# Kernel tuning notes

Measured on AMD Instinct MI355X. Metric: run time of the kernel, lower is better.

The kernel has to match this reference:

```python
import jax, jax.numpy as jnp
import numpy as np

B, S, C, D, K = 8, 1024, 8192, 256, 512
FREEDOM = 0.1

def setup_inputs() -> dict:
    key = jax.random.key(0)
    k1, k2, k3 = jax.random.split(key, 3)
    concept_seq = jax.random.uniform(k1, (B, S, C), dtype=jnp.float32)
    concept_emb = jax.random.uniform(k2, (C, D), dtype=jnp.float32)  # nn.Parameter(torch.rand(max_c+1, d_model))
    centroid_emb = jax.random.uniform(k3, (K, D), dtype=jnp.float32)
    return {"concept_seq": concept_seq, "concept_emb": concept_emb,
            "centroid_emb": centroid_emb, "domain": 0}

def reference(concept_seq, concept_emb, centroid_emb, domain):
    # normalize multi-hot rows by their count (rows summing to 0 use count=1)
    cnt = jnp.sum(concept_seq, axis=-1, keepdims=True)
    cnt = jnp.where(cnt == 0, jnp.ones_like(cnt), cnt)
    cs = concept_seq / cnt
    # weighted embedding sum: [B,S,C] @ [C,D] -> [B,S,D]
    e_free = jnp.einsum('bsc,cd->bsd', cs, concept_emb)
    # nearest centroid (argmin of cdist == argmin of squared distance)
    flat = e_free.reshape(-1, D)                               # [B*S, D]
    d2 = (jnp.sum(flat * flat, axis=1, keepdims=True)
          - 2.0 * flat @ centroid_emb.T
          + jnp.sum(centroid_emb * centroid_emb, axis=1))      # [B*S, K]
    idx = jnp.argmin(d2, axis=1)                               # [B*S]
    e_cent = centroid_emb[idx].reshape(e_free.shape)           # [B,S,D]
    return e_free * FREEDOM + e_cent * (1.0 - FREEDOM)
```

## Files before the change

kernel.cpp:

```cpp
#include <hip/hip_runtime.h>


typedef unsigned short u16;
typedef unsigned int   u32;
using bf16x8 = __attribute__((ext_vector_type(8))) short;
using f32x4  = __attribute__((ext_vector_type(4))) float;

#define MFMA_B16(A,B,C) __builtin_amdgcn_mfma_f32_16x16x32_bf16((A),(B),(C),0,0,0)

static __device__ __forceinline__ u16 f2bf(float f){
  u32 u = __builtin_bit_cast(u32, f);
  u += 0x7FFFu + ((u >> 16) & 1u);
  return (u16)(u >> 16);
}
static __device__ __forceinline__ float bf2f(u16 h){
  u32 u = ((u32)h) << 16;
  return __builtin_bit_cast(float, u);
}
static __device__ __forceinline__ void split2(float va, float vb, u32& hw, u32& lw){
  u16 ha = f2bf(va), hb = f2bf(vb);
  hw = (u32)ha | ((u32)hb << 16);
  lw = (u32)f2bf(va - bf2f(ha)) | ((u32)f2bf(vb - bf2f(hb)) << 16);
}

#define SZ_PART    (4UL*8192UL*256UL*4UL)
#define OFF_CNT    (SZ_PART)
#define SZ_CNT     (4UL*8192UL*4UL)
#define OFF_BHI    (OFF_CNT + SZ_CNT)
#define SZ_BHI     (8192UL*256UL*2UL)
#define OFF_BLO    (OFF_BHI + SZ_BHI)
#define OFF_CTHI   (OFF_BLO + SZ_BHI)
#define SZ_CT      (512UL*256UL*2UL)
#define OFF_CTLO   (OFF_CTHI + SZ_CT)
#define OFF_CNORM  (OFF_CTLO + SZ_CT)

__global__ __launch_bounds__(256) void ce_prep(
    const float* __restrict__ emb, const float* __restrict__ cent,
    u16* __restrict__ Bhi, u16* __restrict__ Blo,
    u16* __restrict__ CThi, u16* __restrict__ CTlo,
    double* __restrict__ cnormd)
{
  const int b = blockIdx.x, t = threadIdx.x;
  const int l = t & 63;
  const int lr = l & 15, lk = l >> 4;
  if (b < 1024) {
    const int g  = b * 4 + (t >> 6);
    const int nt = g >> 8, ksg = g & 255;
    u32 hw[4], lw[4];
    #pragma unroll
    for (int p = 0; p < 4; ++p) {
      float va = emb[(size_t)(ksg*32 + lk*8 + 2*p    )*256 + nt*16 + lr];
      float vb = emb[(size_t)(ksg*32 + lk*8 + 2*p + 1)*256 + nt*16 + lr];
      split2(va, vb, hw[p], lw[p]);
    }
    const size_t fi = ((size_t)nt*256 + ksg)*64 + l;
    *(uint4*)(Bhi + fi*8) = make_uint4(hw[0],hw[1],hw[2],hw[3]);
    *(uint4*)(Blo + fi*8) = make_uint4(lw[0],lw[1],lw[2],lw[3]);
  } else if (b < 1088) {
    const int g  = (b - 1024) * 4 + (t >> 6);
    const int nt = g >> 3, ksg = g & 7;
    u32 hw[4], lw[4];
    #pragma unroll
    for (int p = 0; p < 4; ++p) {
      float va = cent[(size_t)(nt*16 + lr)*256 + ksg*32 + lk*8 + 2*p    ] - 0.5f;
      float vb = cent[(size_t)(nt*16 + lr)*256 + ksg*32 + lk*8 + 2*p + 1] - 0.5f;
      split2(va, vb, hw[p], lw[p]);
    }
    const size_t fi = ((size_t)nt*8 + ksg)*64 + l;
    *(uint4*)(CThi + fi*8) = make_uint4(hw[0],hw[1],hw[2],hw[3]);
    *(uint4*)(CTlo + fi*8) = make_uint4(lw[0],lw[1],lw[2],lw[3]);
  } else {
    const int row = (b - 1088)*8 + (t >> 5);
    const int h = t & 31;
    double s = 0.0;
    #pragma unroll
    for (int j = 0; j < 8; ++j) {
      float x = cent[(size_t)row*256 + h*8 + j] - 0.5f;
      s += (double)x * (double)x;
    }
    #pragma unroll
    for (int off = 16; off > 0; off >>= 1) s += __shfl_xor(s, off);
    if (h == 0) cnormd[row] = s;
  }
}

__global__ __launch_bounds__(512) void ce_gemm(
    const float* __restrict__ seq,
    const u16* __restrict__ Bhi, const u16* __restrict__ Blo,
    float* __restrict__ part, float* __restrict__ cntpart)
{
  __shared__ char Ah[128*128];
  __shared__ char Al[128*128];
  __shared__ float cred[128][4];

  const int t   = threadIdx.x;
  const int blk = blockIdx.x;
  const int mt  = blk >> 2;
  const int ks  = blk & 3;
  const size_t rowBase = (size_t)mt * 128;
  const int ar  = t >> 2;
  const int ac4 = t & 3;
  const float* aptr = seq + (rowBase + ar) * 8192 + (size_t)ks * 2048 + ac4 * 16;

  const int w = t >> 6, l = t & 63;
  const int wm = w >> 2, wn = w & 3;
  const int lr = l & 15, lk = l >> 4;

  f32x4 acc[4][4];
  #pragma unroll
  for (int i = 0; i < 4; ++i)
    #pragma unroll
    for (int j = 0; j < 4; ++j) acc[i][j] = (f32x4){0.f,0.f,0.f,0.f};

  float csum = 0.f;
  float4 areg[4];
  #pragma unroll
  for (int i = 0; i < 4; ++i) areg[i] = *(const float4*)(aptr + i*4);

  for (int step = 0; step < 32; ++step) {
    __syncthreads();
    const int ksg0 = ks*64 + step*2;
    bf16x8 bh[2][4], bl[2][4];
    #pragma unroll
    for (int ksub = 0; ksub < 2; ++ksub)
      #pragma unroll
      for (int ni = 0; ni < 4; ++ni) {
        const size_t fi = (((size_t)(wn*4 + ni))*256 + (ksg0 + ksub))*64 + l;
        bh[ksub][ni] = *(const bf16x8*)(Bhi + fi*8);
        bl[ksub][ni] = *(const bf16x8*)(Blo + fi*8);
      }
    float v[16];
    #pragma unroll
    for (int i = 0; i < 4; ++i) {
      v[4*i] = areg[i].x; v[4*i+1] = areg[i].y; v[4*i+2] = areg[i].z; v[4*i+3] = areg[i].w;
    }
    #pragma unroll
    for (int i = 0; i < 16; ++i) csum += v[i];
    #pragma unroll
    for (int chunk = 0; chunk < 2; ++chunk) {
      u32 hw[4], lw[4];
      #pragma unroll
      for (int p = 0; p < 4; ++p) split2(v[chunk*8 + 2*p], v[chunk*8 + 2*p + 1], hw[p], lw[p]);
      const int slot = ac4*2 + chunk;
      const int off  = ar*128 + ((slot ^ (ar & 7)) << 4);
      *(uint4*)(Ah + off) = make_uint4(hw[0],hw[1],hw[2],hw[3]);
      *(uint4*)(Al + off) = make_uint4(lw[0],lw[1],lw[2],lw[3]);
    }
    if (step < 31) {
      aptr += 64;
      #pragma unroll
      for (int i = 0; i < 4; ++i) areg[i] = *(const float4*)(aptr + i*4);
    }
    __syncthreads();
    #pragma unroll
    for (int ksub = 0; ksub < 2; ++ksub) {
      bf16x8 ah[4], alo[4];
      #pragma unroll
      for (int mi = 0; mi < 4; ++mi) {
        const int row = wm*64 + mi*16 + lr;
        const int off = row*128 + (((ksub*4 + lk) ^ (row & 7)) << 4);
        ah[mi]  = *(const bf16x8*)(Ah + off);
        alo[mi] = *(const bf16x8*)(Al + off);
      }
      #pragma unroll
      for (int mi = 0; mi < 4; ++mi)
        #pragma unroll
        for (int ni = 0; ni < 4; ++ni) {
          acc[mi][ni] = MFMA_B16(ah[mi],  bh[ksub][ni], acc[mi][ni]);
          acc[mi][ni] = MFMA_B16(alo[mi], bh[ksub][ni], acc[mi][ni]);
          acc[mi][ni] = MFMA_B16(ah[mi],  bl[ksub][ni], acc[mi][ni]);
        }
    }
  }
  cred[ar][ac4] = csum;
  __syncthreads();
  if (t < 128) {
    float c = cred[t][0] + cred[t][1] + cred[t][2] + cred[t][3];
    cntpart[(size_t)ks*8192 + rowBase + t] = c;
  }
  float* pbase = part + ((size_t)ks*8192 + rowBase)*256;
  #pragma unroll
  for (int mi = 0; mi < 4; ++mi)
    #pragma unroll
    for (int ni = 0; ni < 4; ++ni) {
      const int col = wn*64 + ni*16 + lr;
      #pragma unroll
      for (int rr = 0; rr < 4; ++rr) {
        const int row = wm*64 + mi*16 + lk*4 + rr;
        pbase[(size_t)row*256 + col] = acc[mi][ni][rr];
      }
    }
}

__global__ __launch_bounds__(256) void ce_cent(
    const float* __restrict__ part, const float* __restrict__ cntpart,
    const u16* __restrict__ CThi, const u16* __restrict__ CTlo,
    const double* __restrict__ cnormd, const float* __restrict__ cent,
    float* __restrict__ out)
{
  __shared__ float eL[32][256];
  __shared__ char Eh[32*512];
  __shared__ char El[32*512];
  __shared__ float GL[32][512];
  __shared__ float cntL[32];
  __shared__ float enred[32][8];
  __shared__ float enL[32];

  const int t = threadIdx.x;
  const size_t rb = (size_t)blockIdx.x * 32;
  const int r  = t >> 3;
  const int c0 = (t & 7) * 32;

  if (t < 32) {
    float s = 0.f;
    #pragma unroll
    for (int p = 0; p < 4; ++p) s += cntpart[(size_t)p*8192 + rb + t];
    cntL[t] = (s == 0.f) ? 1.f : s;
  }
  __syncthreads();
  const float inv = 1.0f / cntL[r];
  float en = 0.f;
  #pragma unroll
  for (int jp = 0; jp < 4; ++jp) {
    float e8[8];
    #pragma unroll
    for (int q = 0; q < 2; ++q) {
      const float* p0 = part + (rb + r)*256 + c0 + jp*8 + q*4;
      float4 s0 = *(const float4*)(p0);
      float4 s1 = *(const float4*)(p0 + 2097152);
      float4 s2 = *(const float4*)(p0 + 2*2097152);
      float4 s3 = *(const float4*)(p0 + 3*2097152);
      float4 e4;
      e4.x = (s0.x + s1.x + s2.x + s3.x) * inv;
      e4.y = (s0.y + s1.y + s2.y + s3.y) * inv;
      e4.z = (s0.z + s1.z + s2.z + s3.z) * inv;
      e4.w = (s0.w + s1.w + s2.w + s3.w) * inv;
      *(float4*)&eL[r][c0 + jp*8 + q*4] = e4;
      e8[q*4+0] = e4.x; e8[q*4+1] = e4.y; e8[q*4+2] = e4.z; e8[q*4+3] = e4.w;
    }
    u32 hw[4], lw[4];
    #pragma unroll
    for (int p = 0; p < 4; ++p) {
      float va = e8[2*p] - 0.5f, vb = e8[2*p+1] - 0.5f;
      split2(va, vb, hw[p], lw[p]);
      en += va*va + vb*vb;
    }
    const int slot = (t & 7)*4 + jp;
    const int off  = r*512 + ((slot ^ (r & 7)) << 4);
    *(uint4*)(Eh + off) = make_uint4(hw[0],hw[1],hw[2],hw[3]);
    *(uint4*)(El + off) = make_uint4(lw[0],lw[1],lw[2],lw[3]);
  }
  enred[r][t & 7] = en;
  __syncthreads();
  if (t < 32) {
    float s = 0.f;
    #pragma unroll
    for (int j = 0; j < 8; ++j) s += enred[t][j];
    enL[t] = s;
  }
  const int w = t >> 6, l = t & 63, lr = l & 15, lk = l >> 4;
  f32x4 acc[2][8];
  #pragma unroll
  for (int i = 0; i < 2; ++i)
    #pragma unroll
    for (int j = 0; j < 8; ++j) acc[i][j] = (f32x4){0.f,0.f,0.f,0.f};
  #pragma unroll
  for (int ksub = 0; ksub < 8; ++ksub) {
    bf16x8 ah[2], alo[2];
    #pragma unroll
    for (int mi = 0; mi < 2; ++mi) {
      const int row = mi*16 + lr;
      const int off = row*512 + (((ksub*4 + lk) ^ (row & 7)) << 4);
      ah[mi]  = *(const bf16x8*)(Eh + off);
      alo[mi] = *(const bf16x8*)(El + off);
    }
    bf16x8 bh[8], bl[8];
    #pragma unroll
    for (int ni = 0; ni < 8; ++ni) {
      const size_t fi = (((size_t)(w*8 + ni))*8 + ksub)*64 + l;
      bh[ni] = *(const bf16x8*)(CThi + fi*8);
      bl[ni] = *(const bf16x8*)(CTlo + fi*8);
    }
    #pragma unroll
    for (int mi = 0; mi < 2; ++mi)
      #pragma unroll
      for (int ni = 0; ni < 8; ++ni) {
        acc[mi][ni] = MFMA_B16(ah[mi],  bh[ni], acc[mi][ni]);
        acc[mi][ni] = MFMA_B16(alo[mi], bh[ni], acc[mi][ni]);
        acc[mi][ni] = MFMA_B16(ah[mi],  bl[ni], acc[mi][ni]);
      }
  }
  #pragma unroll
  for (int mi = 0; mi < 2; ++mi)
    #pragma unroll
    for (int ni = 0; ni < 8; ++ni)
      #pragma unroll
      for (int rr = 0; rr < 4; ++rr)
        GL[mi*16 + lk*4 + rr][w*128 + ni*16 + lr] = acc[mi][ni][rr];
  __syncthreads();
  for (int i = 0; i < 8; ++i) {
    const int row = w*8 + i;
    const double en_ = (double)enL[row];
    double best = 1e300; int bk = 0;
    #pragma unroll
    for (int jj = 0; jj < 8; ++jj) {
      const int k = jj*64 + l;
      const double d2 = en_ + cnormd[k] - 2.0*(double)GL[row][k];
      if (d2 < best) { best = d2; bk = k; }
    }
    #pragma unroll
    for (int off = 32; off > 0; off >>= 1) {
      const double ov = __shfl_xor(best, off);
      const int   ok = __shfl_xor(bk, off);
      if (ov < best || (ov == best && ok < bk)) { best = ov; bk = ok; }
    }
    const float* crow = cent + (size_t)bk*256;
    float4 ef = *(const float4*)&eL[row][l*4];
    float4 cf = *(const float4*)(crow + l*4);
    float4 o;
    o.x = 0.1f*ef.x + 0.9f*cf.x;
    o.y = 0.1f*ef.y + 0.9f*cf.y;
    o.z = 0.1f*ef.z + 0.9f*cf.z;
    o.w = 0.1f*ef.w + 0.9f*cf.w;
    *(float4*)(out + (rb + row)*256 + l*4) = o;
  }
}

extern "C" void kernel_launch(void* const* d_in, const int* in_sizes, int n_in,
                              void* d_out, int out_size, void* d_ws, size_t ws_size,
                              hipStream_t stream) {
  const float* seq  = (const float*)d_in[0];
  const float* emb  = (const float*)d_in[1];
  const float* cent = (const float*)d_in[2];
  float* out = (float*)d_out;
  char* ws = (char*)d_ws;

  float*  part    = (float*) (ws);
  float*  cntpart = (float*) (ws + OFF_CNT);
  u16*    Bhi     = (u16*)   (ws + OFF_BHI);
  u16*    Blo     = (u16*)   (ws + OFF_BLO);
  u16*    CThi    = (u16*)   (ws + OFF_CTHI);
  u16*    CTlo    = (u16*)   (ws + OFF_CTLO);
  double* cnormd  = (double*)(ws + OFF_CNORM);

  hipLaunchKernelGGL(ce_prep, dim3(1152), dim3(256), 0, stream,
                     emb, cent, Bhi, Blo, CThi, CTlo, cnormd);
  hipLaunchKernelGGL(ce_gemm, dim3(256), dim3(512), 0, stream,
                     seq, Bhi, Blo, part, cntpart);
  hipLaunchKernelGGL(ce_cent, dim3(256), dim3(256), 0, stream,
                     part, cntpart, CThi, CTlo, cnormd, cent, out);
}
```

Baseline: 158.6 us.

## Halve GEMM row tile, double-buffer LDS staging, and double grid size

The streaming GEMM now uses 64-row tiles instead of 128, so the grid grows from 256 to 512 blocks. Each wave covers all 64 rows and 32 columns. The bf16 hi/lo staging of the A operand in LDS is double-buffered, so the next chunk is converted and stored while MFMAs run on the current one, with one barrier per step instead of two. The goal is better latency hiding and more blocks in flight on the memory-bound read of the large input. The cost is that each block re-reads the B operand fragments for fewer rows, doubling total B traffic.

```diff
diff --git a/kernel.cpp b/kernel.cpp
--- a/kernel.cpp
+++ b/kernel.cpp
@@ -84,109 +84,120 @@
   }
 }
 
-__global__ __launch_bounds__(512) void ce_gemm(
+__global__ __launch_bounds__(512, 4) void ce_gemm(
     const float* __restrict__ seq,
     const u16* __restrict__ Bhi, const u16* __restrict__ Blo,
     float* __restrict__ part, float* __restrict__ cntpart)
 {
-  __shared__ char Ah[128*128];
-  __shared__ char Al[128*128];
-  __shared__ float cred[128][4];
+  __shared__ char Ah[2][64*128];
+  __shared__ char Al[2][64*128];
+  __shared__ float cred[64][8];
 
   const int t   = threadIdx.x;
   const int blk = blockIdx.x;
   const int mt  = blk >> 2;
   const int ks  = blk & 3;
-  const size_t rowBase = (size_t)mt * 128;
-  const int ar  = t >> 2;
-  const int ac4 = t & 3;
-  const float* aptr = seq + (rowBase + ar) * 8192 + (size_t)ks * 2048 + ac4 * 16;
+  const size_t rowBase = (size_t)mt * 64;
+  const int ar  = t >> 3;
+  const int ac  = t & 7;
+  const float* aptr = seq + (rowBase + ar) * 8192 + (size_t)ks * 2048 + ac * 8;
 
   const int w = t >> 6, l = t & 63;
-  const int wm = w >> 2, wn = w & 3;
   const int lr = l & 15, lk = l >> 4;
 
-  f32x4 acc[4][4];
+  f32x4 acc[4][2];
   #pragma unroll
   for (int i = 0; i < 4; ++i)
     #pragma unroll
-    for (int j = 0; j < 4; ++j) acc[i][j] = (f32x4){0.f,0.f,0.f,0.f};
+    for (int j = 0; j < 2; ++j) acc[i][j] = (f32x4){0.f,0.f,0.f,0.f};
 
   float csum = 0.f;
-  float4 areg[4];
-  #pragma unroll
-  for (int i = 0; i < 4; ++i) areg[i] = *(const float4*)(aptr + i*4);
+  float4 areg0, areg1;
+  areg0 = *(const float4*)(aptr);
+  areg1 = *(const float4*)(aptr + 4);
+
+  {
+    float v[8] = {areg0.x, areg0.y, areg0.z, areg0.w, areg1.x, areg1.y, areg1.z, areg1.w};
+    #pragma unroll
+    for (int i = 0; i < 8; ++i) csum += v[i];
+    u32 hw[4], lw[4];
+    #pragma unroll
+    for (int p = 0; p < 4; ++p) split2(v[2*p], v[2*p+1], hw[p], lw[p]);
+    const int off = ar*128 + ((ac ^ (ar & 7)) << 4);
+    *(uint4*)(Ah[0] + off) = make_uint4(hw[0],hw[1],hw[2],hw[3]);
+    *(uint4*)(Al[0] + off) = make_uint4(lw[0],lw[1],lw[2],lw[3]);
+  }
+  aptr += 64;
+  areg0 = *(const float4*)(aptr);
+  areg1 = *(const float4*)(aptr + 4);
+  __syncthreads();
 
   for (int step = 0; step < 32; ++step) {
-    __syncthreads();
+    const int cur = step & 1;
     const int ksg0 = ks*64 + step*2;
-    bf16x8 bh[2][4], bl[2][4];
+    bf16x8 bh[2][2], bl[2][2];
     #pragma unroll
     for (int ksub = 0; ksub < 2; ++ksub)
       #pragma unroll
-      for (int ni = 0; ni < 4; ++ni) {
-        const size_t fi = (((size_t)(wn*4 + ni))*256 + (ksg0 + ksub))*64 + l;
+      for (int ni = 0; ni < 2; ++ni) {
+        const size_t fi = (((size_t)(w*2 + ni))*256 + (ksg0 + ksub))*64 + l;
         bh[ksub][ni] = *(const bf16x8*)(Bhi + fi*8);
         bl[ksub][ni] = *(const bf16x8*)(Blo + fi*8);
       }
-    float v[16];
-    #pragma unroll
-    for (int i = 0; i < 4; ++i) {
-      v[4*i] = areg[i].x; v[4*i+1] = areg[i].y; v[4*i+2] = areg[i].z; v[4*i+3] = areg[i].w;
-    }
-    #pragma unroll
-    for (int i = 0; i < 16; ++i) csum += v[i];
-    #pragma unroll
-    for (int chunk = 0; chunk < 2; ++chunk) {
+    if (step < 31) {
+      float v[8] = {areg0.x, areg0.y, areg0.z, areg0.w, areg1.x, areg1.y, areg1.z, areg1.w};
+      #pragma unroll
+      for (int i = 0; i < 8; ++i) csum += v[i];
       u32 hw[4], lw[4];
       #pragma unroll
-      for (int p = 0; p < 4; ++p) split2(v[chunk*8 + 2*p], v[chunk*8 + 2*p + 1], hw[p], lw[p]);
-      const int slot = ac4*2 + chunk;
-      const int off  = ar*128 + ((slot ^ (ar & 7)) << 4);
-      *(uint4*)(Ah + off) = make_uint4(hw[0],hw[1],hw[2],hw[3]);
-      *(uint4*)(Al + off) = make_uint4(lw[0],lw[1],lw[2],lw[3]);
-    }
-    if (step < 31) {
-      aptr += 64;
-      #pragma unroll
-      for (int i = 0; i < 4; ++i) areg[i] = *(const float4*)(aptr + i*4);
-    }
-    __syncthreads();
+      for (int p = 0; p < 4; ++p) split2(v[2*p], v[2*p+1], hw[p], lw[p]);
+      const int off = ar*128 + ((ac ^ (ar & 7)) << 4);
+      *(uint4*)(Ah[cur^1] + off) = make_uint4(hw[0],hw[1],hw[2],hw[3]);
+      *(uint4*)(Al[cur^1] + off) = make_uint4(lw[0],lw[1],lw[2],lw[3]);
+      if (step < 30) {
+        aptr += 64;
+        areg0 = *(const float4*)(aptr);
+        areg1 = *(const float4*)(aptr + 4);
+      }
+    }
     #pragma unroll
     for (int ksub = 0; ksub < 2; ++ksub) {
       bf16x8 ah[4], alo[4];
       #pragma unroll
       for (int mi = 0; mi < 4; ++mi) {
-        const int row = wm*64 + mi*16 + lr;
+        const int row = mi*16 + lr;
         const int off = row*128 + (((ksub*4 + lk) ^ (row & 7)) << 4);
-        ah[mi]  = *(const bf16x8*)(Ah + off);
-        alo[mi] = *(const bf16x8*)(Al + off);
+        ah[mi]  = *(const bf16x8*)(Ah[cur] + off);
+        alo[mi] = *(const bf16x8*)(Al[cur] + off);
       }
       #pragma unroll
       for (int mi = 0; mi < 4; ++mi)
         #pragma unroll
-        for (int ni = 0; ni < 4; ++ni) {
+        for (int ni = 0; ni < 2; ++ni) {
           acc[mi][ni] = MFMA_B16(ah[mi],  bh[ksub][ni], acc[mi][ni]);
           acc[mi][ni] = MFMA_B16(alo[mi], bh[ksub][ni], acc[mi][ni]);
           acc[mi][ni] = MFMA_B16(ah[mi],  bl[ksub][ni], acc[mi][ni]);
         }
     }
-  }
-  cred[ar][ac4] = csum;
-  __syncthreads();
-  if (t < 128) {
-    float c = cred[t][0] + cred[t][1] + cred[t][2] + cred[t][3];
+    __syncthreads();
+  }
+  cred[ar][ac] = csum;
+  __syncthreads();
+  if (t < 64) {
+    float c = 0.f;
+    #pragma unroll
+    for (int j = 0; j < 8; ++j) c += cred[t][j];
     cntpart[(size_t)ks*8192 + rowBase + t] = c;
   }
   float* pbase = part + ((size_t)ks*8192 + rowBase)*256;
   #pragma unroll
   for (int mi = 0; mi < 4; ++mi)
     #pragma unroll
-    for (int ni = 0; ni < 4; ++ni) {
-      const int col = wn*64 + ni*16 + lr;
+    for (int ni = 0; ni < 2; ++ni) {
+      const int col = w*32 + ni*16 + lr;
       #pragma unroll
       for (int rr = 0; rr < 4; ++rr) {
-        const int row = wm*64 + mi*16 + lk*4 + rr;
+        const int row = mi*16 + lk*4 + rr;
         pbase[(size_t)row*256 + col] = acc[mi][ni][rr];
       }
     }
@@ -345,7 +356,7 @@
 
   hipLaunchKernelGGL(ce_prep, dim3(1152), dim3(256), 0, stream,
                      emb, cent, Bhi, Blo, CThi, CTlo, cnormd);
-  hipLaunchKernelGGL(ce_gemm, dim3(256), dim3(512), 0, stream,
+  hipLaunchKernelGGL(ce_gemm, dim3(512), dim3(512), 0, stream,
                      seq, Bhi, Blo, part, cntpart);
   hipLaunchKernelGGL(ce_cent, dim3(256), dim3(256), 0, stream,
                      part, cntpart, CThi, CTlo, cnormd, cent, out);
```

New measurement: 147.2 us. 7.2% less time.
